# Kernel optimization log

Hardware: AMD Instinct MI355X
Metric: run time of the kernel (lower is better)

Reference implementation:

```python
import jax, jax.numpy as jnp
import numpy as np

N_NODES = 20000
N_REL = 8
N_EDGES = 320000
IN_DIM, HID_DIM, OUT_DIM = 1280, 512, 256


def _rgcn_layer(x, W, root, bias, src, dst, etype):
    """PyG RGCNConv with num_bases=None, aggr='mean' (mean per (node, relation)).
    x: [N, in], W: [R, in, out], root: [in, out], bias: [out].
    """
    n = x.shape[0]
    # per-(dst, relation) in-degree for relation-wise mean
    key = dst * N_REL + etype  # [E]
    counts = jax.ops.segment_sum(jnp.ones(etype.shape, x.dtype), key,
                                 num_segments=n * N_REL)
    deg = jnp.maximum(counts[key], 1.0)  # [E]
    # transform once per relation, then gather per edge
    H = jnp.einsum('ni,rio->rno', x, W)          # [R, N, out]
    msg = H[etype, src] / deg[:, None]           # [E, out]
    agg = jax.ops.segment_sum(msg, dst, num_segments=n)  # [N, out]
    return agg + x @ root + bias


def setup_inputs() -> dict:
    key = jax.random.key(0)
    ks = jax.random.split(key, 9)
    x = jax.random.normal(ks[0], (N_NODES, IN_DIM), dtype=jnp.float32)
    edge_index = jax.random.randint(ks[1], (2, N_EDGES), 0, N_NODES, dtype=jnp.int32)
    edge_type = jax.random.randint(ks[2], (N_EDGES,), 0, N_REL, dtype=jnp.int32)
    s1 = 1.0 / np.sqrt(IN_DIM)
    s2 = 1.0 / np.sqrt(HID_DIM)
    return {
        'x': x,
        'edge_index': edge_index,
        'edge_type': edge_type,
        'W1': jax.random.normal(ks[3], (N_REL, IN_DIM, HID_DIM), dtype=jnp.float32) * s1,
        'root1': jax.random.normal(ks[4], (IN_DIM, HID_DIM), dtype=jnp.float32) * s1,
        'b1': jnp.zeros((HID_DIM,), dtype=jnp.float32),
        'W2': jax.random.normal(ks[5], (N_REL, HID_DIM, OUT_DIM), dtype=jnp.float32) * s2,
        'root2': jax.random.normal(ks[6], (HID_DIM, OUT_DIM), dtype=jnp.float32) * s2,
        'b2': jnp.zeros((OUT_DIM,), dtype=jnp.float32),
    }


def reference(x, edge_index, edge_type, W1, root1, b1, W2, root2, b2):
    src, dst = edge_index[0], edge_index[1]
    h = _rgcn_layer(x, W1, root1, b1, src, dst, edge_type)
    h = jax.nn.relu(h)
    # dropout is identity in eval mode
    out = _rgcn_layer(h, W2, root2, b2, src, dst, edge_type)
    return out
```

## Files before the change

### kernel.cpp

```cpp
#include <hip/hip_runtime.h>
#include <hip/hip_bf16.h>

#define N_REL 8

typedef unsigned short ushort_t;
typedef unsigned int uint_t;
typedef __attribute__((ext_vector_type(8))) short short8;
typedef __attribute__((ext_vector_type(4))) float floatx4;

static __device__ __forceinline__ ushort_t f2bf(float f) {
    union { float f; unsigned u; } v; v.f = f;
    unsigned r = v.u + 0x7fff + ((v.u >> 16) & 1);
    return (ushort_t)(r >> 16);
}

typedef __attribute__((address_space(1))) void glob_void;
typedef __attribute__((address_space(3))) void lds_void;

static __device__ __forceinline__ void load_lds16(const void* g, void* l) {
    __builtin_amdgcn_global_load_lds((glob_void*)g, (lds_void*)l, 16, 0, 0);
}

static __device__ __forceinline__ void stage_half(const ushort_t* __restrict__ g,
                                                  int row0, int rmax, int K, int k0,
                                                  ushort_t* lds, int w, int l) {
    const int rl = l >> 3;
    const int gc = ((l & 7) ^ rl) * 8;
#pragma unroll
    for (int s = 0; s < 2; ++s) {
        int r = row0 + s * 64 + w * 8 + rl;
        r = r < rmax ? r : rmax - 1;
        load_lds16(g + (size_t)r * K + k0 + gc, lds + (s * 64 + w * 8) * 64);
    }
}


__global__ __launch_bounds__(256) void hist_kernel(const int* __restrict__ dst,
                                                   const int* __restrict__ et,
                                                   int* __restrict__ cnt, int E) {
    int e = blockIdx.x * blockDim.x + threadIdx.x;
    if (e < E) atomicAdd(&cnt[dst[e] * N_REL + et[e]], 1);
}

__global__ __launch_bounds__(256) void scan1(const int* __restrict__ cnt,
                                             int* __restrict__ off,
                                             int* __restrict__ bsum, int nk) {
    __shared__ int s[256];
    int t = threadIdx.x;
    int k = blockIdx.x * 256 + t;
    int v = k < nk ? cnt[k] : 0;
    s[t] = v; __syncthreads();
    for (int d = 1; d < 256; d <<= 1) {
        int x = (t >= d) ? s[t - d] : 0;
        __syncthreads(); s[t] += x; __syncthreads();
    }
    if (k < nk) off[k] = s[t] - v;
    if (t == 255) bsum[blockIdx.x] = s[255];
}

__global__ __launch_bounds__(1024) void scan2(int* __restrict__ bsum, int nb) {
    __shared__ int s[1024];
    int t = threadIdx.x;
    int v = t < nb ? bsum[t] : 0;
    s[t] = v; __syncthreads();
    for (int d = 1; d < 1024; d <<= 1) {
        int x = (t >= d) ? s[t - d] : 0;
        __syncthreads(); s[t] += x; __syncthreads();
    }
    if (t < nb) bsum[t] = s[t] - v;
}

__global__ __launch_bounds__(256) void scan3(int* __restrict__ off,
                                             const int* __restrict__ bsum,
                                             int* __restrict__ cursor,
                                             int nk) {
    int k = blockIdx.x * 256 + threadIdx.x;
    if (k >= nk) return;
    int o = off[k] + bsum[k >> 8];
    off[k] = o;
    cursor[k] = o;
}

__global__ __launch_bounds__(256) void scatter_desc(const int* __restrict__ dst,
                                                    const int* __restrict__ et,
                                                    const int* __restrict__ src,
                                                    const int* __restrict__ cnt,
                                                    int* __restrict__ cursor,
                                                    uint2* __restrict__ edesc, int E) {
    int e = blockIdx.x * blockDim.x + threadIdx.x;
    if (e < E) {
        int key = dst[e] * N_REL + et[e];
        int pos = atomicAdd(&cursor[key], 1);
        float inv = 1.0f / (float)cnt[key];
        edesc[pos] = make_uint2((uint_t)src[e] | ((uint_t)et[e] << 27),
                                __float_as_uint(inv));
    }
}


__global__ __launch_bounds__(256) void cast_bf16(const float* __restrict__ in,
                                                 ushort_t* __restrict__ out, long n) {
    long idx = ((long)blockIdx.x * blockDim.x + threadIdx.x) * 4;
    if (idx + 4 <= n) {
        float4 v = *(const float4*)(in + idx);
        ushort_t o[4] = {f2bf(v.x), f2bf(v.y), f2bf(v.z), f2bf(v.w)};
        *(uint2*)(out + idx) = *(const uint2*)o;
    } else {
        for (; idx < n; ++idx) out[idx] = f2bf(in[idx]);
    }
}

__global__ __launch_bounds__(256) void transpose_cast(const float* __restrict__ in,
                                                      ushort_t* __restrict__ out,
                                                      int K, int N) {
    __shared__ float tile[32][33];
    const float* inp = in + (size_t)blockIdx.z * K * N;
    ushort_t* outp = out + (size_t)blockIdx.z * K * N;
    int n0 = blockIdx.x * 32, k0 = blockIdx.y * 32;
    int tx = threadIdx.x & 31, ty = threadIdx.x >> 5;
#pragma unroll
    for (int s = 0; s < 4; ++s)
        tile[ty + 8 * s][tx] = inp[(size_t)(k0 + ty + 8 * s) * N + n0 + tx];
    __syncthreads();
#pragma unroll
    for (int s = 0; s < 4; ++s)
        outp[(size_t)(n0 + ty + 8 * s) * K + k0 + tx] = f2bf(tile[tx][ty + 8 * s]);
}


#define STAGE_A(b, h, ktx) stage_half(A, bm + (h) * 128, M, K, ((ktx) << 6), &sh.st[(b)][0][(h)][0], w, l)
#define STAGE_B(b, h, ktx) stage_half(Bt, bn + (h) * 128, N, K, ((ktx) << 6), &sh.st[(b)][1][(h)][0], w, l)

#define LOAD_A(b, qm)                                                          \
    {                                                                          \
        const ushort_t* pa_ = &sh.st[(b)][0][(qm)][0];                         \
        _Pragma("unroll") for (int i_ = 0; i_ < 4; ++i_) {                     \
            const int r_ = wm * 64 + i_ * 16 + l16;                            \
            _Pragma("unroll") for (int kk_ = 0; kk_ < 2; ++kk_) {              \
                const int ch_ = (kk_ * 4 + quad) ^ (r_ & 7);                   \
                areg[i_][kk_] = *(const short8*)&pa_[r_ * 64 + ch_ * 8];       \
            }                                                                  \
        }                                                                      \
    }

#define LOAD_B(b, qn)                                                          \
    {                                                                          \
        const ushort_t* pb_ = &sh.st[(b)][1][(qn)][0];                         \
        _Pragma("unroll") for (int j_ = 0; j_ < 2; ++j_) {                     \
            const int r_ = wn * 32 + j_ * 16 + l16;                            \
            _Pragma("unroll") for (int kk_ = 0; kk_ < 2; ++kk_) {              \
                const int ch_ = (kk_ * 4 + quad) ^ (r_ & 7);                   \
                breg[(qn)][j_][kk_] = *(const short8*)&pb_[r_ * 64 + ch_ * 8]; \
            }                                                                  \
        }                                                                      \
    }

#define MFMA_Q(qm, qn)                                                              \
    _Pragma("unroll") for (int i_ = 0; i_ < 4; ++i_)                                \
        _Pragma("unroll") for (int j_ = 0; j_ < 2; ++j_)                            \
            _Pragma("unroll") for (int kk_ = 0; kk_ < 2; ++kk_)                     \
                acc[(qm)][(qn)][i_][j_] = __builtin_amdgcn_mfma_f32_16x16x32_bf16(  \
                    areg[i_][kk_], breg[(qn)][j_][kk_], acc[(qm)][(qn)][i_][j_], 0, 0, 0);

#define PHASE_SYNC()                                                           \
    __builtin_amdgcn_s_barrier();                                              \
    asm volatile("s_waitcnt lgkmcnt(0)" ::: "memory");                         \
    __builtin_amdgcn_sched_barrier(0)

#define WINDOW(kt, b)                                                          \
    {                                                                          \
                                 \
        LOAD_A(b, 0);                                                          \
        LOAD_B(b, 0);                                                          \
        if ((kt) + 1 < nkt) STAGE_A((b) ^ 1, 1, (kt) + 1);                     \
        PHASE_SYNC();                                                          \
        __builtin_amdgcn_s_setprio(1);                                         \
        MFMA_Q(0, 0);                                                          \
        __builtin_amdgcn_s_setprio(0);                                         \
        __builtin_amdgcn_s_barrier();                                          \
                        \
        LOAD_B(b, 1);                                                          \
        if ((kt) + 2 < nkt) STAGE_A(b, 0, (kt) + 2);                           \
        PHASE_SYNC();                                                          \
        __builtin_amdgcn_s_setprio(1);                                         \
        MFMA_Q(0, 1);                                                          \
        __builtin_amdgcn_s_setprio(0);                                         \
        __builtin_amdgcn_s_barrier();                                          \
                            \
        LOAD_A(b, 1);                                                          \
        if ((kt) + 2 < nkt) STAGE_B(b, 0, (kt) + 2);                           \
        PHASE_SYNC();                                                          \
        __builtin_amdgcn_s_setprio(1);                                         \
        MFMA_Q(1, 0);                                                          \
        __builtin_amdgcn_s_setprio(0);                                         \
        __builtin_amdgcn_s_barrier();                                          \
           \
        if ((kt) + 2 < nkt) {                                                  \
            STAGE_B(b, 1, (kt) + 2);                                           \
            asm volatile("s_waitcnt vmcnt(6)" ::: "memory");                   \
        } else {                                                               \
            asm volatile("s_waitcnt vmcnt(0)" ::: "memory");  \
        }                                                                      \
        __builtin_amdgcn_s_barrier();                                          \
        __builtin_amdgcn_sched_barrier(0);                                     \
        __builtin_amdgcn_s_setprio(1);                                         \
        MFMA_Q(1, 1);                                                          \
        __builtin_amdgcn_s_setprio(0);                                         \
        __builtin_amdgcn_s_barrier();                                          \
    }

__global__ __launch_bounds__(512, 2) void gemm256(const ushort_t* __restrict__ A,
                                                  const ushort_t* __restrict__ Bt,
                                                  ushort_t* __restrict__ C,
                                                  int M, int K, int N) {
    __shared__ union {
        __align__(16) ushort_t st[2][2][2][128 * 64];
        __align__(16) ushort_t c[256 * 256];
    } sh;

    const int t = threadIdx.x;
    const int l = t & 63;
    const int w = t >> 6;
    const int wm = w >> 2, wn = w & 3;
    const int quad = l >> 4, l16 = l & 15;

    const int nx = gridDim.x;
    const int nwg = nx * gridDim.y;
    const int orig = blockIdx.y * nx + blockIdx.x;
    const int q8 = nwg >> 3, r8 = nwg & 7;
    const int xcd = orig & 7;
    const int wgid = ((xcd < r8) ? xcd * (q8 + 1) : r8 * (q8 + 1) + (xcd - r8) * q8) + (orig >> 3);
    const int bm = (wgid / nx) * 256;
    const int bn = (wgid % nx) * 256;

    const int nkt = K >> 6;

    floatx4 acc[2][2][4][2];
#pragma unroll
    for (int a = 0; a < 2; ++a)
#pragma unroll
        for (int bq = 0; bq < 2; ++bq)
#pragma unroll
            for (int i = 0; i < 4; ++i)
#pragma unroll
                for (int j = 0; j < 2; ++j) acc[a][bq][i][j] = (floatx4)(0.f);

    short8 areg[4][2];
    short8 breg[2][2][2];

    STAGE_A(0, 0, 0); STAGE_B(0, 0, 0); STAGE_B(0, 1, 0); STAGE_A(0, 1, 0);
    STAGE_A(1, 0, 1); STAGE_B(1, 0, 1); STAGE_B(1, 1, 1);
    asm volatile("s_waitcnt vmcnt(6)" ::: "memory");
    __builtin_amdgcn_s_barrier();

    for (int kt = 0; kt < nkt; kt += 2) {
        WINDOW(kt, 0);
        WINDOW(kt + 1, 1);
    }

    __syncthreads();
#pragma unroll
    for (int qm = 0; qm < 2; ++qm)
#pragma unroll
        for (int qn = 0; qn < 2; ++qn)
#pragma unroll
            for (int i = 0; i < 4; ++i)
#pragma unroll
                for (int j = 0; j < 2; ++j) {
                    const int rl = qm * 128 + wm * 64 + i * 16 + quad * 4;
                    const int cl = qn * 128 + wn * 32 + j * 16 + l16;
#pragma unroll
                    for (int rg = 0; rg < 4; ++rg)
                        sh.c[(rl + rg) * 256 + cl] = f2bf(acc[qm][qn][i][j][rg]);
                }
    __syncthreads();
#pragma unroll
    for (int sw = 0; sw < 16; ++sw) {
        const int idx = sw * 512 + t;
        const int row = idx >> 5;
        const int ch = (idx & 31) * 8;
        const int grow = bm + row;
        if (grow < M)
            *(uint4*)(C + (size_t)grow * N + bn + ch) = *(const uint4*)&sh.c[row * 256 + ch];
    }
}

#undef STAGE_A
#undef STAGE_B
#undef LOAD_A
#undef LOAD_B
#undef MFMA_Q
#undef PHASE_SYNC
#undef WINDOW


template <int DIM, bool L1MODE>
__global__ __launch_bounds__(64) void segsum_wave(const ushort_t* __restrict__ H,
                                                  const float* __restrict__ bias,
                                                  const int* __restrict__ off,
                                                  const int* __restrict__ cnt,
                                                  const uint2* __restrict__ edesc,
                                                  ushort_t* __restrict__ outb,
                                                  float* __restrict__ outf) {
    constexpr int VPT = DIM / 64;
    constexpr int WPT = VPT / 2;
    const int d = blockIdx.x;
    const int t = threadIdx.x;
    const int hs = (N_REL + 1) * DIM;

    const int base = off[d * N_REL];
    const int total = off[d * N_REL + N_REL - 1] + cnt[d * N_REL + N_REL - 1] - base;

    float acc[VPT];
    {
        uint_t rw[WPT];
        const ushort_t* hp = H + (size_t)d * hs + VPT * t;
        if constexpr (WPT == 4) *(uint4*)rw = *(const uint4*)hp;
        else                    *(uint2*)rw = *(const uint2*)hp;
#pragma unroll
        for (int jq = 0; jq < WPT; ++jq) {
            acc[2 * jq]     = __uint_as_float(rw[jq] << 16);
            acc[2 * jq + 1] = __uint_as_float(rw[jq] & 0xffff0000u);
        }
        const float* bp = bias + VPT * t;
#pragma unroll
        for (int jq = 0; jq < VPT; ++jq) acc[jq] += bp[jq];
    }

    const uint2* __restrict__ ed = edesc + base;
    const ushort_t* __restrict__ Hlane = H + VPT * t;

    int p = 0;
    while (p + 8 <= total) {
        uint2 dsc[8];
#pragma unroll
        for (int q = 0; q < 8; ++q) dsc[q] = ed[p + q];
        uint_t val[8][WPT];
#pragma unroll
        for (int q = 0; q < 8; ++q) {
            const uint_t pk = dsc[q].x;
            const size_t s = pk & 0x07ffffffu;
            const int r = pk >> 27;
            const ushort_t* hp = Hlane + s * hs + (r + 1) * DIM;
            if constexpr (WPT == 4) *(uint4*)val[q] = *(const uint4*)hp;
            else                    *(uint2*)val[q] = *(const uint2*)hp;
        }
#pragma unroll
        for (int q = 0; q < 8; ++q) {
            const float inv = __uint_as_float(dsc[q].y);
#pragma unroll
            for (int jq = 0; jq < WPT; ++jq) {
                acc[2 * jq]     += inv * __uint_as_float(val[q][jq] << 16);
                acc[2 * jq + 1] += inv * __uint_as_float(val[q][jq] & 0xffff0000u);
            }
        }
        p += 8;
    }
    for (; p < total; ++p) {
        const uint2 dq = ed[p];
        const uint_t pk = dq.x;
        const size_t s = pk & 0x07ffffffu;
        const int r = pk >> 27;
        const float inv = __uint_as_float(dq.y);
        uint_t vw[WPT];
        const ushort_t* hp = Hlane + s * hs + (r + 1) * DIM;
        if constexpr (WPT == 4) *(uint4*)vw = *(const uint4*)hp;
        else                    *(uint2*)vw = *(const uint2*)hp;
#pragma unroll
        for (int jq = 0; jq < WPT; ++jq) {
            acc[2 * jq]     += inv * __uint_as_float(vw[jq] << 16);
            acc[2 * jq + 1] += inv * __uint_as_float(vw[jq] & 0xffff0000u);
        }
    }

    if constexpr (L1MODE) {
        ushort_t ob[VPT];
#pragma unroll
        for (int jq = 0; jq < VPT; ++jq) ob[jq] = f2bf(fmaxf(acc[jq], 0.f));
        if constexpr (WPT == 4)
            *(uint4*)(outb + (size_t)d * DIM + VPT * t) = *(const uint4*)ob;
        else
            *(uint2*)(outb + (size_t)d * DIM + VPT * t) = *(const uint2*)ob;
    } else {
        float* op = outf + (size_t)d * DIM + VPT * t;
#pragma unroll
        for (int jq = 0; jq < WPT; ++jq)
            *(float2*)(op + 2 * jq) = make_float2(acc[2 * jq], acc[2 * jq + 1]);
    }
}


extern "C" void kernel_launch(void* const* d_in, const int* in_sizes, int n_in,
                              void* d_out, int out_size, void* d_ws, size_t ws_size,
                              hipStream_t stream) {
    const float* x     = (const float*)d_in[0];
    const int*   eidx  = (const int*)d_in[1];
    const int*   etype = (const int*)d_in[2];
    const float* W1    = (const float*)d_in[3];
    const float* root1 = (const float*)d_in[4];
    const float* b1    = (const float*)d_in[5];
    const float* W2    = (const float*)d_in[6];
    const float* root2 = (const float*)d_in[7];
    const float* b2    = (const float*)d_in[8];
    float* out = (float*)d_out;

    const int IN_DIM = 1280, HID_DIM = 512, OUT_DIM = 256;
    const int E = in_sizes[2];
    const int N = in_sizes[0] / IN_DIM;
    const int NK = N * N_REL;
    const int* srcs = eidx;
    const int* dsts = eidx + E;

    char* ws = (char*)d_ws;
    size_t offb = 0;
    auto alloc = [&](size_t bytes) { void* p = ws + offb; offb += (bytes + 255) & ~(size_t)255; return p; };
    int*      cnt    = (int*)alloc((size_t)NK * 4);
    int*      off    = (int*)alloc((size_t)NK * 4);
    int*      cursor = (int*)alloc((size_t)NK * 4);
    int*      bsum   = (int*)alloc(1024 * 4);
    uint2*    edesc  = (uint2*)alloc((size_t)E * 8);
    ushort_t* x_bf   = (ushort_t*)alloc((size_t)N * IN_DIM * 2);
    ushort_t* rW1t   = (ushort_t*)alloc((size_t)(N_REL + 1) * IN_DIM * HID_DIM * 2);
    ushort_t* r1t    = rW1t;
    ushort_t* W1t    = rW1t + (size_t)HID_DIM * IN_DIM;
    ushort_t* rW2t   = (ushort_t*)alloc((size_t)(N_REL + 1) * HID_DIM * OUT_DIM * 2);
    ushort_t* r2t    = rW2t;
    ushort_t* W2t    = rW2t + (size_t)OUT_DIM * HID_DIM;
    ushort_t* Hb     = (ushort_t*)alloc((size_t)N * (N_REL + 1) * HID_DIM * 2);
    ushort_t* hb_bf  = x_bf;
    (void)ws_size;

    const int nb = (NK + 255) / 256;

    hipMemsetAsync(cnt, 0, (size_t)NK * 4, stream);
    hist_kernel<<<(E + 255) / 256, 256, 0, stream>>>(dsts, etype, cnt, E);
    scan1<<<nb, 256, 0, stream>>>(cnt, off, bsum, NK);
    scan2<<<1, 1024, 0, stream>>>(bsum, nb);
    scan3<<<nb, 256, 0, stream>>>(off, bsum, cursor, NK);
    scatter_desc<<<(E + 255) / 256, 256, 0, stream>>>(dsts, etype, srcs, cnt, cursor, edesc, E);

    {
        long n = (long)N * IN_DIM;
        cast_bf16<<<(unsigned)((n / 4 + 255) / 256), 256, 0, stream>>>(x, x_bf, n);
    }
    transpose_cast<<<dim3(HID_DIM / 32, IN_DIM / 32, 1), 256, 0, stream>>>(root1, r1t, IN_DIM, HID_DIM);
    transpose_cast<<<dim3(HID_DIM / 32, IN_DIM / 32, N_REL), 256, 0, stream>>>(W1, W1t, IN_DIM, HID_DIM);
    transpose_cast<<<dim3(OUT_DIM / 32, HID_DIM / 32, 1), 256, 0, stream>>>(root2, r2t, HID_DIM, OUT_DIM);
    transpose_cast<<<dim3(OUT_DIM / 32, HID_DIM / 32, N_REL), 256, 0, stream>>>(W2, W2t, HID_DIM, OUT_DIM);

    const int mb = (N + 255) / 256;

    {
        const int NTOT = (N_REL + 1) * HID_DIM;
        gemm256<<<dim3(NTOT / 256, mb), 512, 0, stream>>>(x_bf, rW1t, Hb, N, IN_DIM, NTOT);
        segsum_wave<512, true><<<N, 64, 0, stream>>>(Hb, b1, off, cnt, edesc, hb_bf, nullptr);
    }

    {
        const int NTOT = (N_REL + 1) * OUT_DIM;
        gemm256<<<dim3(NTOT / 256, mb), 512, 0, stream>>>(hb_bf, rW2t, Hb, N, HID_DIM, NTOT);
        segsum_wave<256, false><<<N, 64, 0, stream>>>(Hb, b2, off, cnt, edesc, nullptr, out);
    }
}
```

Baseline: 612.7 us.

## Make GEMM persistent with next-tile prefetch during epilogue; widen segment-sum blocks

```diff
diff --git a/kernel.cpp b/kernel.cpp
--- a/kernel.cpp
+++ b/kernel.cpp
@@ -199,7 +199,7 @@
             STAGE_B(b, 1, (kt) + 2);                                           \
             asm volatile("s_waitcnt vmcnt(6)" ::: "memory");                   \
         } else {                                                               \
-            asm volatile("s_waitcnt vmcnt(0)" ::: "memory");  \
+            asm volatile("s_waitcnt vmcnt(0)" ::: "memory");   \
         }                                                                      \
         __builtin_amdgcn_s_barrier();                                          \
         __builtin_amdgcn_sched_barrier(0);                                     \
@@ -209,13 +209,14 @@
         __builtin_amdgcn_s_barrier();                                          \
     }
 
-__global__ __launch_bounds__(512, 2) void gemm256(const ushort_t* __restrict__ A,
-                                                  const ushort_t* __restrict__ Bt,
-                                                  ushort_t* __restrict__ C,
-                                                  int M, int K, int N) {
-    __shared__ union {
+__global__ __launch_bounds__(512, 2) void gemm256p2(const ushort_t* __restrict__ A,
+                                                    const ushort_t* __restrict__ Bt,
+                                                    ushort_t* __restrict__ C,
+                                                    int M, int K, int N,
+                                                    int ntiles, int nx) {
+    __shared__ struct {
         __align__(16) ushort_t st[2][2][2][128 * 64];
-        __align__(16) ushort_t c[256 * 256];
+        __align__(16) ushort_t c2[32 * 256];
     } sh;
 
     const int t = threadIdx.x;
@@ -224,27 +225,20 @@
     const int wm = w >> 2, wn = w & 3;
     const int quad = l >> 4, l16 = l & 15;
 
-    const int nx = gridDim.x;
-    const int nwg = nx * gridDim.y;
-    const int orig = blockIdx.y * nx + blockIdx.x;
-    const int q8 = nwg >> 3, r8 = nwg & 7;
-    const int xcd = orig & 7;
-    const int wgid = ((xcd < r8) ? xcd * (q8 + 1) : r8 * (q8 + 1) + (xcd - r8) * q8) + (orig >> 3);
-    const int bm = (wgid / nx) * 256;
-    const int bn = (wgid % nx) * 256;
-
     const int nkt = K >> 6;
+    const int q8 = ntiles >> 3, r8 = ntiles & 7;
+
+    int T = blockIdx.x;
+    if (T >= ntiles) return;
+    int bm, bn, bm2 = 0, bn2 = 0;
+    {
+        const int xcd = T & 7;
+        const int wgid = ((xcd < r8) ? xcd * (q8 + 1) : r8 * (q8 + 1) + (xcd - r8) * q8) + (T >> 3);
+        bm = (wgid / nx) * 256;
+        bn = (wgid % nx) * 256;
+    }
 
     floatx4 acc[2][2][4][2];
-#pragma unroll
-    for (int a = 0; a < 2; ++a)
-#pragma unroll
-        for (int bq = 0; bq < 2; ++bq)
-#pragma unroll
-            for (int i = 0; i < 4; ++i)
-#pragma unroll
-                for (int j = 0; j < 2; ++j) acc[a][bq][i][j] = (floatx4)(0.f);
-
     short8 areg[4][2];
     short8 breg[2][2][2];
 
@@ -253,35 +247,76 @@
     asm volatile("s_waitcnt vmcnt(6)" ::: "memory");
     __builtin_amdgcn_s_barrier();
 
-    for (int kt = 0; kt < nkt; kt += 2) {
-        WINDOW(kt, 0);
-        WINDOW(kt + 1, 1);
-    }
-
-    __syncthreads();
-#pragma unroll
-    for (int qm = 0; qm < 2; ++qm)
-#pragma unroll
-        for (int qn = 0; qn < 2; ++qn)
-#pragma unroll
-            for (int i = 0; i < 4; ++i)
-#pragma unroll
-                for (int j = 0; j < 2; ++j) {
-                    const int rl = qm * 128 + wm * 64 + i * 16 + quad * 4;
-                    const int cl = qn * 128 + wn * 32 + j * 16 + l16;
-#pragma unroll
-                    for (int rg = 0; rg < 4; ++rg)
-                        sh.c[(rl + rg) * 256 + cl] = f2bf(acc[qm][qn][i][j][rg]);
-                }
-    __syncthreads();
-#pragma unroll
-    for (int sw = 0; sw < 16; ++sw) {
-        const int idx = sw * 512 + t;
-        const int row = idx >> 5;
-        const int ch = (idx & 31) * 8;
-        const int grow = bm + row;
-        if (grow < M)
-            *(uint4*)(C + (size_t)grow * N + bn + ch) = *(const uint4*)&sh.c[row * 256 + ch];
+    while (true) {
+#pragma unroll
+        for (int a = 0; a < 2; ++a)
+#pragma unroll
+            for (int bq = 0; bq < 2; ++bq)
+#pragma unroll
+                for (int i = 0; i < 4; ++i)
+#pragma unroll
+                    for (int j = 0; j < 2; ++j) acc[a][bq][i][j] = (floatx4)(0.f);
+
+        for (int kt = 0; kt < nkt; kt += 2) {
+            WINDOW(kt, 0);
+            WINDOW(kt + 1, 1);
+        }
+
+        const int Tn = T + gridDim.x;
+        const bool have_next = Tn < ntiles;
+        if (have_next) {
+            const int xcd = Tn & 7;
+            const int wgid = ((xcd < r8) ? xcd * (q8 + 1) : r8 * (q8 + 1) + (xcd - r8) * q8) + (Tn >> 3);
+            bm2 = (wgid / nx) * 256;
+            bn2 = (wgid % nx) * 256;
+            stage_half(A, bm2,       M, K, 0,  &sh.st[0][0][0][0], w, l);
+            stage_half(Bt, bn2,      N, K, 0,  &sh.st[0][1][0][0], w, l);
+            stage_half(Bt, bn2 + 128, N, K, 0, &sh.st[0][1][1][0], w, l);
+            stage_half(A, bm2 + 128, M, K, 0,  &sh.st[0][0][1][0], w, l);
+            stage_half(A, bm2,       M, K, 64, &sh.st[1][0][0][0], w, l);
+            stage_half(Bt, bn2,      N, K, 64, &sh.st[1][1][0][0], w, l);
+            stage_half(Bt, bn2 + 128, N, K, 64, &sh.st[1][1][1][0], w, l);
+        }
+
+#pragma unroll
+        for (int pc = 0; pc < 8; ++pc) {
+            const int qm = pc >> 2;
+            const int wmSel = (pc >> 1) & 1;
+            const int ih = pc & 1;
+            if (wm == wmSel) {
+#pragma unroll
+                for (int qn = 0; qn < 2; ++qn)
+#pragma unroll
+                    for (int io = 0; io < 2; ++io)
+#pragma unroll
+                        for (int j = 0; j < 2; ++j) {
+                            const int cl = qn * 128 + wn * 32 + j * 16 + l16;
+                            const int i = ih * 2 + io;
+#pragma unroll
+                            for (int rg = 0; rg < 4; ++rg)
+                                sh.c2[(io * 16 + quad * 4 + rg) * 256 + cl] =
+                                    f2bf(acc[qm][qn][i][j][rg]);
+                        }
+            }
+            asm volatile("s_waitcnt lgkmcnt(0)" ::: "memory");
+            __builtin_amdgcn_s_barrier();
+#pragma unroll
+            for (int it = 0; it < 2; ++it) {
+                const int idx = it * 512 + t;
+                const int rl = idx >> 5;
+                const int ch8 = (idx & 31) * 8;
+                const int grow = bm + pc * 32 + rl;
+                if (grow < M)
+                    *(uint4*)(C + (size_t)grow * N + bn + ch8) =
+                        *(const uint4*)&sh.c2[rl * 256 + ch8];
+            }
+            __builtin_amdgcn_s_barrier();
+        }
+
+        if (!have_next) break;
+        T = Tn; bm = bm2; bn = bn2;
+        asm volatile("s_waitcnt vmcnt(6)" ::: "memory");
+        __builtin_amdgcn_s_barrier();
     }
 }
 
@@ -295,14 +330,14 @@
 
 
 template <int DIM, bool L1MODE>
-__global__ __launch_bounds__(64) void segsum_wave(const ushort_t* __restrict__ H,
-                                                  const float* __restrict__ bias,
-                                                  const int* __restrict__ off,
-                                                  const int* __restrict__ cnt,
-                                                  const uint2* __restrict__ edesc,
-                                                  ushort_t* __restrict__ outb,
-                                                  float* __restrict__ outf) {
-    constexpr int VPT = DIM / 64;
+__global__ __launch_bounds__(128) void segsum_node(const ushort_t* __restrict__ H,
+                                                   const float* __restrict__ bias,
+                                                   const int* __restrict__ off,
+                                                   const int* __restrict__ cnt,
+                                                   const uint2* __restrict__ edesc,
+                                                   ushort_t* __restrict__ outb,
+                                                   float* __restrict__ outf) {
+    constexpr int VPT = DIM / 128;
     constexpr int WPT = VPT / 2;
     const int d = blockIdx.x;
     const int t = threadIdx.x;
@@ -315,8 +350,8 @@
     {
         uint_t rw[WPT];
         const ushort_t* hp = H + (size_t)d * hs + VPT * t;
-        if constexpr (WPT == 4) *(uint4*)rw = *(const uint4*)hp;
-        else                    *(uint2*)rw = *(const uint2*)hp;
+        if constexpr (WPT == 2) *(uint2*)rw = *(const uint2*)hp;
+        else                    rw[0] = *(const uint_t*)hp;
 #pragma unroll
         for (int jq = 0; jq < WPT; ++jq) {
             acc[2 * jq]     = __uint_as_float(rw[jq] << 16);
@@ -330,11 +365,16 @@
     const uint2* __restrict__ ed = edesc + base;
     const ushort_t* __restrict__ Hlane = H + VPT * t;
 
-    int p = 0;
-    while (p + 8 <= total) {
+    for (int p = 0; p < total; p += 8) {
         uint2 dsc[8];
 #pragma unroll
-        for (int q = 0; q < 8; ++q) dsc[q] = ed[p + q];
+        for (int q = 0; q < 8; ++q) {
+            const int idx = (p + q < total) ? p + q : total - 1;
+            dsc[q] = ed[idx];
+        }
+#pragma unroll
+        for (int q = 0; q < 8; ++q)
+            if (p + q >= total) dsc[q].y = 0u;
         uint_t val[8][WPT];
 #pragma unroll
         for (int q = 0; q < 8; ++q) {
@@ -342,8 +382,8 @@
             const size_t s = pk & 0x07ffffffu;
             const int r = pk >> 27;
             const ushort_t* hp = Hlane + s * hs + (r + 1) * DIM;
-            if constexpr (WPT == 4) *(uint4*)val[q] = *(const uint4*)hp;
-            else                    *(uint2*)val[q] = *(const uint2*)hp;
+            if constexpr (WPT == 2) *(uint2*)val[q] = *(const uint2*)hp;
+            else                    val[q][0] = *(const uint_t*)hp;
         }
 #pragma unroll
         for (int q = 0; q < 8; ++q) {
@@ -354,33 +394,16 @@
                 acc[2 * jq + 1] += inv * __uint_as_float(val[q][jq] & 0xffff0000u);
             }
         }
-        p += 8;
-    }
-    for (; p < total; ++p) {
-        const uint2 dq = ed[p];
-        const uint_t pk = dq.x;
-        const size_t s = pk & 0x07ffffffu;
-        const int r = pk >> 27;
-        const float inv = __uint_as_float(dq.y);
-        uint_t vw[WPT];
-        const ushort_t* hp = Hlane + s * hs + (r + 1) * DIM;
-        if constexpr (WPT == 4) *(uint4*)vw = *(const uint4*)hp;
-        else                    *(uint2*)vw = *(const uint2*)hp;
-#pragma unroll
-        for (int jq = 0; jq < WPT; ++jq) {
-            acc[2 * jq]     += inv * __uint_as_float(vw[jq] << 16);
-            acc[2 * jq + 1] += inv * __uint_as_float(vw[jq] & 0xffff0000u);
-        }
     }
 
     if constexpr (L1MODE) {
         ushort_t ob[VPT];
 #pragma unroll
         for (int jq = 0; jq < VPT; ++jq) ob[jq] = f2bf(fmaxf(acc[jq], 0.f));
-        if constexpr (WPT == 4)
-            *(uint4*)(outb + (size_t)d * DIM + VPT * t) = *(const uint4*)ob;
+        if constexpr (WPT == 2)
+            *(uint2*)(outb + (size_t)d * DIM + VPT * t) = *(const uint2*)ob;
         else
-            *(uint2*)(outb + (size_t)d * DIM + VPT * t) = *(const uint2*)ob;
+            *(uint_t*)(outb + (size_t)d * DIM + VPT * t) = *(const uint_t*)ob;
     } else {
         float* op = outf + (size_t)d * DIM + VPT * t;
 #pragma unroll
@@ -452,13 +475,15 @@
 
     {
         const int NTOT = (N_REL + 1) * HID_DIM;
-        gemm256<<<dim3(NTOT / 256, mb), 512, 0, stream>>>(x_bf, rW1t, Hb, N, IN_DIM, NTOT);
-        segsum_wave<512, true><<<N, 64, 0, stream>>>(Hb, b1, off, cnt, edesc, hb_bf, nullptr);
+        const int nxg = NTOT / 256;
+        gemm256p2<<<256, 512, 0, stream>>>(x_bf, rW1t, Hb, N, IN_DIM, NTOT, mb * nxg, nxg);
+        segsum_node<512, true><<<N, 128, 0, stream>>>(Hb, b1, off, cnt, edesc, hb_bf, nullptr);
     }
 
     {
         const int NTOT = (N_REL + 1) * OUT_DIM;
-        gemm256<<<dim3(NTOT / 256, mb), 512, 0, stream>>>(hb_bf, rW2t, Hb, N, HID_DIM, NTOT);
-        segsum_wave<256, false><<<N, 64, 0, stream>>>(Hb, b2, off, cnt, edesc, nullptr, out);
-    }
-}
+        const int nxg = NTOT / 256;
+        gemm256p2<<<256, 512, 0, stream>>>(hb_bf, rW2t, Hb, N, HID_DIM, NTOT, mb * nxg, nxg);
+        segsum_node<256, false><<<N, 128, 0, stream>>>(Hb, b2, off, cnt, edesc, nullptr, out);
+    }
+}
```

New measurement: 621.2 us. No clear change (+1.4%).
